# Optimization experiments

Hardware: AMD Instinct MI355X
Metric: run time of the kernel (lower is better)

## Reference

```python
import math
import jax, jax.numpy as jnp
import numpy as np

H = 16  # num_attention_heads
D = 64  # attention_head_size
ALPHA = 32.0  # PB-relax alpha


def setup_inputs() -> dict:
    key = jax.random.key(0)
    ks = jax.random.split(key, 8)
    B, S, C = 4, 1024, 1024
    scale = 1.0 / math.sqrt(C)
    return {
        "hidden_states": jax.random.normal(ks[0], (B, S, C), jnp.float32),
        "attention_mask": jnp.zeros((B, 1, 1, S), jnp.float32),
        "rel_pos": jax.random.normal(ks[1], (B, H, S, S), jnp.float32),
        "rel_2d_pos": jax.random.normal(ks[2], (B, H, S, S), jnp.float32),
        "Wq": jax.random.normal(ks[3], (C, C), jnp.float32) * scale,
        "bq": jnp.zeros((C,), jnp.float32),
        "Wk": jax.random.normal(ks[4], (C, C), jnp.float32) * scale,
        "bk": jnp.zeros((C,), jnp.float32),
        "Wv": jax.random.normal(ks[5], (C, C), jnp.float32) * scale,
        "bv": jnp.zeros((C,), jnp.float32),
    }


def _heads(x, B, S):
    # [B,S,C] -> [B,H,S,D]
    return x.reshape(B, S, H, D).transpose(0, 2, 1, 3)


def cogview_softmax(scores):
    # PB-relax: softmax(((s/alpha) - max(s/alpha)) * alpha)
    s = scores / ALPHA
    m = jnp.max(s, axis=-1, keepdims=True)
    return jax.nn.softmax((s - m) * ALPHA, axis=-1)


def reference(hidden_states, attention_mask, rel_pos, rel_2d_pos,
              Wq, bq, Wk, bk, Wv, bv):
    B, S, C = hidden_states.shape
    inv_sqrt_d = 1.0 / math.sqrt(D)
    # torch nn.Linear: y = x @ W.T + b; here W is stored as [out, in]
    q = _heads(hidden_states @ Wq.T + bq, B, S)  # [B,H,S,D]
    k = _heads(hidden_states @ Wk.T + bk, B, S)
    v = _heads(hidden_states @ Wv.T + bv, B, S)

    scores = jnp.einsum('bhqd,bhkd->bhqk', q * inv_sqrt_d, k)
    scores = scores + (rel_pos + rel_2d_pos) * inv_sqrt_d
    scores = scores + attention_mask  # broadcast [B,1,1,S]

    probs = cogview_softmax(scores)  # dropout prob = 0 (eval)
    ctx = jnp.einsum('bhqk,bhkd->bhqd', probs, v)
    ctx = ctx.transpose(0, 2, 1, 3).reshape(B, S, C)
    return ctx
```

## Files before the change

kernel.cpp:

```cpp
#include <hip/hip_runtime.h>
#include <hip/hip_bf16.h>

typedef __attribute__((ext_vector_type(8))) short bf16x8;
typedef __attribute__((ext_vector_type(4))) float f32x4;

#define LDSG(g, l) __builtin_amdgcn_global_load_lds(                      \
    (const __attribute__((address_space(1))) void*)(g),                   \
    (__attribute__((address_space(3))) void*)(l), 16, 0, 0)

#define LOG2E 1.44269504088896f
#define RELSC 0.180336880111112f

__global__ __launch_bounds__(256) void cvt_kernel(
    const float* __restrict__ hs,
    const float* __restrict__ wq, const float* __restrict__ wk,
    const float* __restrict__ wv,
    __hip_bfloat16* __restrict__ hbf, __hip_bfloat16* __restrict__ wbf)
{
  const int NH = (4 * 1024 * 1024) / 4;
  const int NW = (1024 * 1024) / 4;
  int i = blockIdx.x * 256 + threadIdx.x;
  float4 v;
  __hip_bfloat16* dst;
  if (i < NH) {
    v = ((const float4*)hs)[i];
    dst = hbf + (size_t)i * 4;
  } else {
    int j = i - NH;
    int which = j / NW, r = j - which * NW;
    const float* src = which == 0 ? wq : (which == 1 ? wk : wv);
    v = ((const float4*)src)[r];
    dst = wbf + (size_t)j * 4;
  }
  union { ushort4 u; __hip_bfloat16 b[4]; } o;
  o.b[0] = __float2bfloat16(v.x);
  o.b[1] = __float2bfloat16(v.y);
  o.b[2] = __float2bfloat16(v.z);
  o.b[3] = __float2bfloat16(v.w);
  *((ushort4*)dst) = o.u;
}

__global__ __launch_bounds__(256) void qkv_gemm(
    const __hip_bfloat16* __restrict__ A,
    const __hip_bfloat16* __restrict__ W,
    const float* __restrict__ bq, const float* __restrict__ bk,
    const float* __restrict__ bv,
    __hip_bfloat16* __restrict__ qo, __hip_bfloat16* __restrict__ ko,
    __hip_bfloat16* __restrict__ vo)
{
  const int K = 1024;
  __shared__ __hip_bfloat16 As[128 * 64];
  __shared__ __hip_bfloat16 Bs[128 * 64];
  const int bid = blockIdx.x;
  const int bm = bid & 31, bn = bid >> 5;
  const int m0 = bm * 128, n0 = bn * 128;
  const int tid = threadIdx.x, wid = tid >> 6, lane = tid & 63;
  const int wm = wid >> 1, wn = wid & 1;

  f32x4 acc[4][4] = {};

  const int srow = lane >> 3;
  const int schunk = (lane & 7) ^ srow;

  for (int k0 = 0; k0 < K; k0 += 64) {
#pragma unroll
    for (int p = 0; p < 4; ++p) {
      int r = (wid * 4 + p) * 8 + srow;
      LDSG(&A[(size_t)(m0 + r) * K + k0 + schunk * 8], &As[(wid * 4 + p) * 512]);
      LDSG(&W[(size_t)(n0 + r) * K + k0 + schunk * 8], &Bs[(wid * 4 + p) * 512]);
    }
    __syncthreads();
#pragma unroll
    for (int ks = 0; ks < 2; ++ks) {
      bf16x8 af[4], bfr[4];
#pragma unroll
      for (int mi = 0; mi < 4; ++mi) {
        int row = wm * 64 + mi * 16 + (lane & 15);
        int slot = (ks * 4 + (lane >> 4)) ^ (lane & 7);
        af[mi] = *(const bf16x8*)((const char*)As + row * 128 + slot * 16);
      }
#pragma unroll
      for (int ni = 0; ni < 4; ++ni) {
        int row = wn * 64 + ni * 16 + (lane & 15);
        int slot = (ks * 4 + (lane >> 4)) ^ (lane & 7);
        bfr[ni] = *(const bf16x8*)((const char*)Bs + row * 128 + slot * 16);
      }
#pragma unroll
      for (int mi = 0; mi < 4; ++mi)
#pragma unroll
        for (int ni = 0; ni < 4; ++ni)
          acc[mi][ni] = __builtin_amdgcn_mfma_f32_16x16x32_bf16(
              af[mi], bfr[ni], acc[mi][ni], 0, 0, 0);
    }
    __syncthreads();
  }

#pragma unroll
  for (int ni = 0; ni < 4; ++ni) {
    int n = n0 + wn * 64 + ni * 16 + (lane & 15);
    int which = n >> 10;
    int h = (n >> 6) & 15;
    int d = n & 63;
    const float* bias = which == 0 ? bq : (which == 1 ? bk : bv);
    float bval = bias[n & 1023];
    if (which == 0) {
#pragma unroll
      for (int mi = 0; mi < 4; ++mi) {
#pragma unroll
        for (int j = 0; j < 4; ++j) {
          int m = m0 + wm * 64 + mi * 16 + (lane >> 4) * 4 + j;
          int b = m >> 10, s = m & 1023;
          float val = (acc[mi][ni][j] + bval) * RELSC;
          qo[(((size_t)(b * 16 + h) << 10) + s) * 64 + d] = __float2bfloat16(val);
        }
      }
    } else if (which == 1) {
      int dks = d >> 5, dlg = (d >> 3) & 3, de = d & 7;
#pragma unroll
      for (int mi = 0; mi < 4; ++mi) {
#pragma unroll
        for (int j = 0; j < 4; ++j) {
          int m = m0 + wm * 64 + mi * 16 + (lane >> 4) * 4 + j;
          int b = m >> 10, s = m & 1023;
          size_t idx = ((((size_t)(b * 16 + h)) * 16 + (s >> 6)) * 512 +
                        (size_t)((dks * 4 + ((s >> 4) & 3)) * 64 + (s & 15) +
                                 16 * dlg)) * 8 + de;
          ko[idx] = __float2bfloat16(acc[mi][ni][j] + bval);
        }
      }
    } else {
      int dt = d >> 4, dl15 = d & 15;
#pragma unroll
      for (int mi = 0; mi < 4; ++mi) {
        int m = m0 + wm * 64 + mi * 16 + (lane >> 4) * 4;
        int b = m >> 10, k = m & 1023;
        int kt = k >> 6, kks = (k >> 5) & 1, klg = (k >> 3) & 3, ke = k & 7;
        union { ushort4 u; __hip_bfloat16 bb[4]; } o;
#pragma unroll
        for (int j = 0; j < 4; ++j)
          o.bb[j] = __float2bfloat16(acc[mi][ni][j] + bval);
        size_t idx = ((((size_t)(b * 16 + h)) * 16 + kt) * 512 +
                      (size_t)((kks * 4 + dt) * 64 + dl15 + 16 * klg)) * 8 + ke;
        *(ushort4*)&vo[idx] = o.u;
      }
    }
  }
}

__global__ __launch_bounds__(256, 2) void attn_kernel(
    const __hip_bfloat16* __restrict__ qg, const __hip_bfloat16* __restrict__ kf,
    const __hip_bfloat16* __restrict__ vf,
    const float* __restrict__ rel1, const float* __restrict__ rel2,
    const float* __restrict__ mask, float* __restrict__ out)
{
  __shared__ float Rbuf[4][2][2][16][64];
  __shared__ float Ml[1024];
  __shared__ __hip_bfloat16 Ps[4][16 * 64];

  const int bid = blockIdx.x;
  const int bh = bid & 63, qt = bid >> 6;
  const int b = bh >> 4, h = bh & 15;
  const int tid = threadIdx.x, wid = tid >> 6, lane = tid & 63;
  const int lg = lane >> 4, ln15 = lane & 15;
  const int r4 = lane >> 4, c15 = lane & 15;

  const size_t qbase = (size_t)bh << 16;
  const size_t fbase = (size_t)bh << 16;
  const int q0 = qt * 64 + wid * 16;

  {
    float4 mv = *(const float4*)&mask[((size_t)b << 10) + tid * 4];
    float4 sm;
    sm.x = mv.x * LOG2E - 32.0f; sm.y = mv.y * LOG2E - 32.0f;
    sm.z = mv.z * LOG2E - 32.0f; sm.w = mv.w * LOG2E - 32.0f;
    *(float4*)&Ml[tid * 4] = sm;
  }
  __syncthreads();

  bf16x8 qf[2];
  qf[0] = *(const bf16x8*)&qg[qbase + (size_t)(q0 + ln15) * 64 + lg * 8];
  qf[1] = *(const bf16x8*)&qg[qbase + (size_t)(q0 + ln15) * 64 + 32 + lg * 8];

  f32x4 accO[4] = {};
  float lrun = 0.f;

  const float* relw1 = rel1 + ((size_t)bh << 20);
  const float* relw2 = rel2 + ((size_t)bh << 20);

#define STAGE_REL(BUF, KB) do {                                             \
    _Pragma("unroll") for (int p = 0; p < 4; ++p) {                         \
      int rg = 4 * p + r4;                                                  \
      int cg = c15 ^ (rg & 7);                                              \
      LDSG(&relw1[(size_t)(q0 + rg) * 1024 + (KB) + cg * 4],                \
           &Rbuf[wid][BUF][0][4 * p][0]);                                   \
      LDSG(&relw2[(size_t)(q0 + rg) * 1024 + (KB) + cg * 4],                \
           &Rbuf[wid][BUF][1][4 * p][0]);                                   \
    } } while (0)

#define LOAD_K(KF_, KT) do {                                                \
    _Pragma("unroll") for (int i = 0; i < 8; ++i)                           \
      KF_[i] = *(const bf16x8*)&kf[fbase + (size_t)(KT) * 4096 + i * 512 +  \
                                   lane * 8];                               \
    } while (0)

#define LOAD_V(VF_, KT) do {                                                \
    _Pragma("unroll") for (int i = 0; i < 8; ++i)                           \
      VF_[i] = *(const bf16x8*)&vf[fbase + (size_t)(KT) * 4096 + i * 512 +  \
                                   lane * 8];                               \
    } while (0)

#define BODY(BUF, KT, DO_STAGE) do {                                        \
    bf16x8 kfr[8], vfr[8];                                                  \
    LOAD_K(kfr, KT);                                                        \
    LOAD_V(vfr, KT);                                                        \
    __builtin_amdgcn_sched_barrier(0);                                      \
    if (DO_STAGE) STAGE_REL((BUF) ^ 1, ((KT) + 1) * 64);                    \
    __builtin_amdgcn_sched_barrier(0);                                      \
    f32x4 st[4] = {};                                                       \
    _Pragma("unroll") for (int ks = 0; ks < 2; ++ks)                        \
      _Pragma("unroll") for (int ct = 0; ct < 4; ++ct)                      \
        st[ct] = __builtin_amdgcn_mfma_f32_16x16x32_bf16(                   \
            kfr[ks * 4 + ct], qf[ks], st[ct], 0, 0, 0);                     \
    asm volatile("s_waitcnt vmcnt(16)" ::: "memory");                       \
    __builtin_amdgcn_sched_barrier(0);                                      \
    float p[4][4];                                                          \
    _Pragma("unroll") for (int ct = 0; ct < 4; ++ct) {                      \
      int cc = ((ct * 4 + lg) ^ (ln15 & 7)) * 16;                           \
      float4 rv1 = *(const float4*)((const char*)&Rbuf[wid][BUF][0][0][0] + \
                                    ln15 * 256 + cc);                       \
      float4 rv2 = *(const float4*)((const char*)&Rbuf[wid][BUF][1][0][0] + \
                                    ln15 * 256 + cc);                       \
      float4 mv = *(const float4*)&Ml[(KT) * 64 + ct * 16 + lg * 4];        \
      _Pragma("unroll") for (int j = 0; j < 4; ++j) {                       \
        float sv = st[ct][j] +                                              \
                   RELSC * (((const float*)&rv1)[j] +                       \
                            ((const float*)&rv2)[j]) +                      \
                   ((const float*)&mv)[j];                                  \
        float e = __builtin_amdgcn_exp2f(sv);                               \
        p[ct][j] = e; lrun += e;                                            \
      }                                                                     \
    }                                                                       \
    __hip_bfloat16* Pw = &Ps[wid][0];                                       \
    _Pragma("unroll") for (int ct = 0; ct < 4; ++ct) {                      \
      union { ushort4 u; __hip_bfloat16 bb[4]; } w;                         \
      _Pragma("unroll") for (int j = 0; j < 4; ++j)                         \
        w.bb[j] = __float2bfloat16(p[ct][j]);                               \
      *(ushort4*)((char*)Pw + ln15 * 128 +                                  \
                  ((ct * 32 + lg * 8) ^ ((ln15 & 7) << 4))) = w.u;          \
    }                                                                       \
    bf16x8 pt[2];                                                           \
    pt[0] = *(const bf16x8*)((const char*)Pw + ln15 * 128 +                 \
                             ((lg * 16) ^ ((ln15 & 7) << 4)));              \
    pt[1] = *(const bf16x8*)((const char*)Pw + ln15 * 128 +                 \
                             ((64 + lg * 16) ^ ((ln15 & 7) << 4)));         \
    _Pragma("unroll") for (int ks = 0; ks < 2; ++ks)                        \
      _Pragma("unroll") for (int dt = 0; dt < 4; ++dt)                      \
        accO[dt] = __builtin_amdgcn_mfma_f32_16x16x32_bf16(                 \
            vfr[ks * 4 + dt], pt[ks], accO[dt], 0, 0, 0);                   \
  } while (0)

  STAGE_REL(0, 0);

  for (int t = 0; t < 7; ++t) {
    BODY(0, 2 * t, 1);
    BODY(1, 2 * t + 1, 1);
  }
  BODY(0, 14, 1);
  BODY(1, 15, 0);

  lrun += __shfl_xor(lrun, 16, 64);
  lrun += __shfl_xor(lrun, 32, 64);
  float rl = 1.0f / lrun;

#pragma unroll
  for (int dt = 0; dt < 4; ++dt) {
    float4 o;
    o.x = accO[dt][0] * rl;
    o.y = accO[dt][1] * rl;
    o.z = accO[dt][2] * rl;
    o.w = accO[dt][3] * rl;
    *(float4*)&out[((size_t)(b * 1024 + q0 + ln15)) * 1024 + h * 64 +
                   dt * 16 + lg * 4] = o;
  }
}

extern "C" void kernel_launch(void* const* d_in, const int* in_sizes, int n_in,
                              void* d_out, int out_size, void* d_ws,
                              size_t ws_size, hipStream_t stream) {
  const float* hs   = (const float*)d_in[0];
  const float* mask = (const float*)d_in[1];
  const float* rel1 = (const float*)d_in[2];
  const float* rel2 = (const float*)d_in[3];
  const float* Wq   = (const float*)d_in[4];
  const float* bq   = (const float*)d_in[5];
  const float* Wk   = (const float*)d_in[6];
  const float* bk   = (const float*)d_in[7];
  const float* Wv   = (const float*)d_in[8];
  const float* bv   = (const float*)d_in[9];

  char* ws = (char*)d_ws;
  __hip_bfloat16* hbf = (__hip_bfloat16*)(ws);
  __hip_bfloat16* wbf = (__hip_bfloat16*)(ws + 8388608);
  __hip_bfloat16* qb  = (__hip_bfloat16*)(ws + 14680064);
  __hip_bfloat16* kfb = (__hip_bfloat16*)(ws + 23068672);
  __hip_bfloat16* vfb = (__hip_bfloat16*)(ws + 31457280);

  cvt_kernel<<<7168, 256, 0, stream>>>(hs, Wq, Wk, Wv, hbf, wbf);
  qkv_gemm<<<768, 256, 0, stream>>>(hbf, wbf, bq, bk, bv, qb, kfb, vfb);
  attn_kernel<<<1024, 256, 0, stream>>>(qb, kfb, vfb, rel1, rel2, mask,
                                        (float*)d_out);
}
```

Measured before the change: 200.7 us.

## Split attention block into producer waves for rel-pos staging and consumer waves

Doubles the attention block to 512 threads. Four extra producer waves prefetch the rel_pos and rel_2d_pos tiles into double-buffered LDS with async global-to-LDS loads, while the four original waves only do the QK, softmax and PV math. The two groups hand off each 64-key step through a block-wide barrier, replacing the old per-wave software pipeline that issued its own staging loads and waited with a manual vmcnt. The intent is to overlap the heavy fp32 rel-pos streaming with the MFMA and exp work. The trade-offs are a barrier every iteration, and launch bounds of (512, 4) that cap VGPRs tightly, which may cause register spills in the consumer waves.

```diff
diff --git a/kernel.cpp b/kernel.cpp
--- a/kernel.cpp
+++ b/kernel.cpp
@@ -147,7 +147,7 @@
   }
 }
 
-__global__ __launch_bounds__(256, 2) void attn_kernel(
+__global__ __launch_bounds__(512, 4) void attn_kernel(
     const __hip_bfloat16* __restrict__ qg, const __hip_bfloat16* __restrict__ kf,
     const __hip_bfloat16* __restrict__ vf,
     const float* __restrict__ rel1, const float* __restrict__ rel2,
@@ -162,20 +162,52 @@
   const int b = bh >> 4, h = bh & 15;
   const int tid = threadIdx.x, wid = tid >> 6, lane = tid & 63;
   const int lg = lane >> 4, ln15 = lane & 15;
-  const int r4 = lane >> 4, c15 = lane & 15;
 
   const size_t qbase = (size_t)bh << 16;
   const size_t fbase = (size_t)bh << 16;
+
+  {
+    float2 mv = *(const float2*)&mask[((size_t)b << 10) + tid * 2];
+    float2 sm;
+    sm.x = mv.x * LOG2E - 32.0f;
+    sm.y = mv.y * LOG2E - 32.0f;
+    *(float2*)&Ml[tid * 2] = sm;
+  }
+
+  if (wid >= 4) {
+    const int cw = wid - 4;
+    const int q0c = qt * 64 + cw * 16;
+    const int r4 = lane >> 4, c15 = lane & 15;
+    const float* relw1 = rel1 + ((size_t)bh << 20);
+    const float* relw2 = rel2 + ((size_t)bh << 20);
+
+#pragma unroll
+    for (int p = 0; p < 4; ++p) {
+      int rg = 4 * p + r4;
+      int cg = c15 ^ (rg & 7);
+      LDSG(&relw1[(size_t)(q0c + rg) * 1024 + cg * 4], &Rbuf[cw][0][0][4 * p][0]);
+      LDSG(&relw2[(size_t)(q0c + rg) * 1024 + cg * 4], &Rbuf[cw][0][1][4 * p][0]);
+    }
+    __syncthreads();
+
+    for (int t = 0; t < 15; ++t) {
+      int buf = (t + 1) & 1;
+      int kb = (t + 1) * 64;
+#pragma unroll
+      for (int p = 0; p < 4; ++p) {
+        int rg = 4 * p + r4;
+        int cg = c15 ^ (rg & 7);
+        LDSG(&relw1[(size_t)(q0c + rg) * 1024 + kb + cg * 4],
+             &Rbuf[cw][buf][0][4 * p][0]);
+        LDSG(&relw2[(size_t)(q0c + rg) * 1024 + kb + cg * 4],
+             &Rbuf[cw][buf][1][4 * p][0]);
+      }
+      __syncthreads();
+    }
+    return;
+  }
+
   const int q0 = qt * 64 + wid * 16;
-
-  {
-    float4 mv = *(const float4*)&mask[((size_t)b << 10) + tid * 4];
-    float4 sm;
-    sm.x = mv.x * LOG2E - 32.0f; sm.y = mv.y * LOG2E - 32.0f;
-    sm.z = mv.z * LOG2E - 32.0f; sm.w = mv.w * LOG2E - 32.0f;
-    *(float4*)&Ml[tid * 4] = sm;
-  }
-  __syncthreads();
 
   bf16x8 qf[2];
   qf[0] = *(const bf16x8*)&qg[qbase + (size_t)(q0 + ln15) * 64 + lg * 8];
@@ -184,89 +216,69 @@
   f32x4 accO[4] = {};
   float lrun = 0.f;
 
-  const float* relw1 = rel1 + ((size_t)bh << 20);
-  const float* relw2 = rel2 + ((size_t)bh << 20);
-
-#define STAGE_REL(BUF, KB) do {                                             \
-    _Pragma("unroll") for (int p = 0; p < 4; ++p) {                         \
-      int rg = 4 * p + r4;                                                  \
-      int cg = c15 ^ (rg & 7);                                              \
-      LDSG(&relw1[(size_t)(q0 + rg) * 1024 + (KB) + cg * 4],                \
-           &Rbuf[wid][BUF][0][4 * p][0]);                                   \
-      LDSG(&relw2[(size_t)(q0 + rg) * 1024 + (KB) + cg * 4],                \
-           &Rbuf[wid][BUF][1][4 * p][0]);                                   \
-    } } while (0)
-
-#define LOAD_K(KF_, KT) do {                                                \
-    _Pragma("unroll") for (int i = 0; i < 8; ++i)                           \
-      KF_[i] = *(const bf16x8*)&kf[fbase + (size_t)(KT) * 4096 + i * 512 +  \
-                                   lane * 8];                               \
-    } while (0)
-
-#define LOAD_V(VF_, KT) do {                                                \
-    _Pragma("unroll") for (int i = 0; i < 8; ++i)                           \
-      VF_[i] = *(const bf16x8*)&vf[fbase + (size_t)(KT) * 4096 + i * 512 +  \
-                                   lane * 8];                               \
-    } while (0)
-
-#define BODY(BUF, KT, DO_STAGE) do {                                        \
-    bf16x8 kfr[8], vfr[8];                                                  \
-    LOAD_K(kfr, KT);                                                        \
-    LOAD_V(vfr, KT);                                                        \
-    __builtin_amdgcn_sched_barrier(0);                                      \
-    if (DO_STAGE) STAGE_REL((BUF) ^ 1, ((KT) + 1) * 64);                    \
-    __builtin_amdgcn_sched_barrier(0);                                      \
-    f32x4 st[4] = {};                                                       \
-    _Pragma("unroll") for (int ks = 0; ks < 2; ++ks)                        \
-      _Pragma("unroll") for (int ct = 0; ct < 4; ++ct)                      \
-        st[ct] = __builtin_amdgcn_mfma_f32_16x16x32_bf16(                   \
-            kfr[ks * 4 + ct], qf[ks], st[ct], 0, 0, 0);                     \
-    asm volatile("s_waitcnt vmcnt(16)" ::: "memory");                       \
-    __builtin_amdgcn_sched_barrier(0);                                      \
-    float p[4][4];                                                          \
-    _Pragma("unroll") for (int ct = 0; ct < 4; ++ct) {                      \
-      int cc = ((ct * 4 + lg) ^ (ln15 & 7)) * 16;                           \
-      float4 rv1 = *(const float4*)((const char*)&Rbuf[wid][BUF][0][0][0] + \
-                                    ln15 * 256 + cc);                       \
-      float4 rv2 = *(const float4*)((const char*)&Rbuf[wid][BUF][1][0][0] + \
-                                    ln15 * 256 + cc);                       \
-      float4 mv = *(const float4*)&Ml[(KT) * 64 + ct * 16 + lg * 4];        \
-      _Pragma("unroll") for (int j = 0; j < 4; ++j) {                       \
-        float sv = st[ct][j] +                                              \
-                   RELSC * (((const float*)&rv1)[j] +                       \
-                            ((const float*)&rv2)[j]) +                      \
-                   ((const float*)&mv)[j];                                  \
-        float e = __builtin_amdgcn_exp2f(sv);                               \
-        p[ct][j] = e; lrun += e;                                            \
-      }                                                                     \
-    }                                                                       \
-    __hip_bfloat16* Pw = &Ps[wid][0];                                       \
-    _Pragma("unroll") for (int ct = 0; ct < 4; ++ct) {                      \
-      union { ushort4 u; __hip_bfloat16 bb[4]; } w;                         \
-      _Pragma("unroll") for (int j = 0; j < 4; ++j)                         \
-        w.bb[j] = __float2bfloat16(p[ct][j]);                               \
-      *(ushort4*)((char*)Pw + ln15 * 128 +                                  \
-                  ((ct * 32 + lg * 8) ^ ((ln15 & 7) << 4))) = w.u;          \
-    }                                                                       \
-    bf16x8 pt[2];                                                           \
-    pt[0] = *(const bf16x8*)((const char*)Pw + ln15 * 128 +                 \
-                             ((lg * 16) ^ ((ln15 & 7) << 4)));              \
-    pt[1] = *(const bf16x8*)((const char*)Pw + ln15 * 128 +                 \
-                             ((64 + lg * 16) ^ ((ln15 & 7) << 4)));         \
-    _Pragma("unroll") for (int ks = 0; ks < 2; ++ks)                        \
-      _Pragma("unroll") for (int dt = 0; dt < 4; ++dt)                      \
-        accO[dt] = __builtin_amdgcn_mfma_f32_16x16x32_bf16(                 \
-            vfr[ks * 4 + dt], pt[ks], accO[dt], 0, 0, 0);                   \
-  } while (0)
-
-  STAGE_REL(0, 0);
-
-  for (int t = 0; t < 7; ++t) {
-    BODY(0, 2 * t, 1);
-    BODY(1, 2 * t + 1, 1);
-  }
-  BODY(0, 14, 1);
-  BODY(1, 15, 0);
+  __syncthreads();
+
+  for (int t = 0; t < 16; ++t) {
+    bf16x8 kfr[8], vfr[8];
+#pragma unroll
+    for (int i = 0; i < 8; ++i)
+      kfr[i] = *(const bf16x8*)&kf[fbase + (size_t)t * 4096 + i * 512 + lane * 8];
+#pragma unroll
+    for (int i = 0; i < 8; ++i)
+      vfr[i] = *(const bf16x8*)&vf[fbase + (size_t)t * 4096 + i * 512 + lane * 8];
+
+    f32x4 st[4] = {};
+#pragma unroll
+    for (int ks = 0; ks < 2; ++ks)
+#pragma unroll
+      for (int ct = 0; ct < 4; ++ct)
+        st[ct] = __builtin_amdgcn_mfma_f32_16x16x32_bf16(
+            kfr[ks * 4 + ct], qf[ks], st[ct], 0, 0, 0);
+
+    const char* Rb1 = (const char*)&Rbuf[wid][t & 1][0][0][0];
+    const char* Rb2 = (const char*)&Rbuf[wid][t & 1][1][0][0];
+    float p_[4][4];
+#pragma unroll
+    for (int ct = 0; ct < 4; ++ct) {
+      int cc = ((ct * 4 + lg) ^ (ln15 & 7)) * 16;
+      float4 rv1 = *(const float4*)(Rb1 + ln15 * 256 + cc);
+      float4 rv2 = *(const float4*)(Rb2 + ln15 * 256 + cc);
+      float4 mv = *(const float4*)&Ml[t * 64 + ct * 16 + lg * 4];
+#pragma unroll
+      for (int j = 0; j < 4; ++j) {
+        float sv = st[ct][j] +
+                   RELSC * (((const float*)&rv1)[j] + ((const float*)&rv2)[j]) +
+                   ((const float*)&mv)[j];
+        float e = __builtin_amdgcn_exp2f(sv);
+        p_[ct][j] = e;
+        lrun += e;
+      }
+    }
+
+    __hip_bfloat16* Pw = &Ps[wid][0];
+#pragma unroll
+    for (int ct = 0; ct < 4; ++ct) {
+      union { ushort4 u; __hip_bfloat16 bb[4]; } w;
+#pragma unroll
+      for (int j = 0; j < 4; ++j) w.bb[j] = __float2bfloat16(p_[ct][j]);
+      *(ushort4*)((char*)Pw + ln15 * 128 +
+                  ((ct * 32 + lg * 8) ^ ((ln15 & 7) << 4))) = w.u;
+    }
+    bf16x8 pt[2];
+    pt[0] = *(const bf16x8*)((const char*)Pw + ln15 * 128 +
+                             ((lg * 16) ^ ((ln15 & 7) << 4)));
+    pt[1] = *(const bf16x8*)((const char*)Pw + ln15 * 128 +
+                             ((64 + lg * 16) ^ ((ln15 & 7) << 4)));
+
+#pragma unroll
+    for (int ks = 0; ks < 2; ++ks)
+#pragma unroll
+      for (int dt = 0; dt < 4; ++dt)
+        accO[dt] = __builtin_amdgcn_mfma_f32_16x16x32_bf16(
+            vfr[ks * 4 + dt], pt[ks], accO[dt], 0, 0, 0);
+
+    if (t < 15) __syncthreads();
+  }
 
   lrun += __shfl_xor(lrun, 16, 64);
   lrun += __shfl_xor(lrun, 32, 64);
@@ -307,6 +319,6 @@
 
   cvt_kernel<<<7168, 256, 0, stream>>>(hs, Wq, Wk, Wv, hbf, wbf);
   qkv_gemm<<<768, 256, 0, stream>>>(hbf, wbf, bq, bk, bv, qb, kfb, vfb);
-  attn_kernel<<<1024, 256, 0, stream>>>(qb, kfb, vfb, rel1, rel2, mask,
+  attn_kernel<<<1024, 512, 0, stream>>>(qb, kfb, vfb, rel1, rel2, mask,
                                         (float*)d_out);
 }
```

Result: faster. 171.6 us (-14.5%).

## Warp-specialize attention: producer waves stage rel-pos tiles, consumer waves double-buffer K/V

Applied to the files above, without the earlier changes.

The attention block grows to 512 threads. Four producer waves fill the mask table and stream the two relative-position tiles into double-buffered LDS. Four consumer waves run the QK/softmax/PV math, prefetching the next K/V tile into a second register set. The two groups stay in step by matching barrier counts, so rel-pos staging leaves the compute waves' instruction stream. The tighter launch bounds (512 threads, 4 blocks) and the doubled K/V register footprint risk register spills, and LDS size probably caps how many blocks fit per CU.

```diff
diff --git a/kernel.cpp b/kernel.cpp
--- a/kernel.cpp
+++ b/kernel.cpp
@@ -147,7 +147,7 @@
   }
 }
 
-__global__ __launch_bounds__(256, 2) void attn_kernel(
+__global__ __launch_bounds__(512, 4) void attn_kernel(
     const __hip_bfloat16* __restrict__ qg, const __hip_bfloat16* __restrict__ kf,
     const __hip_bfloat16* __restrict__ vf,
     const float* __restrict__ rel1, const float* __restrict__ rel2,
@@ -162,89 +162,108 @@
   const int b = bh >> 4, h = bh & 15;
   const int tid = threadIdx.x, wid = tid >> 6, lane = tid & 63;
   const int lg = lane >> 4, ln15 = lane & 15;
-  const int r4 = lane >> 4, c15 = lane & 15;
 
   const size_t qbase = (size_t)bh << 16;
   const size_t fbase = (size_t)bh << 16;
+
+  if (wid >= 4) {
+    const int cw = wid - 4;
+    const int q0c = qt * 64 + cw * 16;
+    const int r4 = lane >> 4, c15 = lane & 15;
+    const float* relw1 = rel1 + ((size_t)bh << 20);
+    const float* relw2 = rel2 + ((size_t)bh << 20);
+
+    {
+      int i = cw * 64 + lane;
+      float4 mv = *(const float4*)&mask[((size_t)b << 10) + i * 4];
+      float4 sm;
+      sm.x = mv.x * LOG2E - 32.0f; sm.y = mv.y * LOG2E - 32.0f;
+      sm.z = mv.z * LOG2E - 32.0f; sm.w = mv.w * LOG2E - 32.0f;
+      *(float4*)&Ml[i * 4] = sm;
+    }
+
+#pragma unroll
+    for (int p = 0; p < 4; ++p) {
+      int rg = 4 * p + r4;
+      int cg = c15 ^ (rg & 7);
+      LDSG(&relw1[(size_t)(q0c + rg) * 1024 + cg * 4], &Rbuf[cw][0][0][4 * p][0]);
+      LDSG(&relw2[(size_t)(q0c + rg) * 1024 + cg * 4], &Rbuf[cw][0][1][4 * p][0]);
+    }
+    __syncthreads();
+
+    for (int t = 0; t < 15; ++t) {
+      int buf = (t + 1) & 1;
+      int kb = (t + 1) * 64;
+#pragma unroll
+      for (int p = 0; p < 4; ++p) {
+        int rg = 4 * p + r4;
+        int cg = c15 ^ (rg & 7);
+        LDSG(&relw1[(size_t)(q0c + rg) * 1024 + kb + cg * 4],
+             &Rbuf[cw][buf][0][4 * p][0]);
+        LDSG(&relw2[(size_t)(q0c + rg) * 1024 + kb + cg * 4],
+             &Rbuf[cw][buf][1][4 * p][0]);
+      }
+      __syncthreads();
+    }
+    return;
+  }
+
   const int q0 = qt * 64 + wid * 16;
-
-  {
-    float4 mv = *(const float4*)&mask[((size_t)b << 10) + tid * 4];
-    float4 sm;
-    sm.x = mv.x * LOG2E - 32.0f; sm.y = mv.y * LOG2E - 32.0f;
-    sm.z = mv.z * LOG2E - 32.0f; sm.w = mv.w * LOG2E - 32.0f;
-    *(float4*)&Ml[tid * 4] = sm;
-  }
-  __syncthreads();
 
   bf16x8 qf[2];
   qf[0] = *(const bf16x8*)&qg[qbase + (size_t)(q0 + ln15) * 64 + lg * 8];
   qf[1] = *(const bf16x8*)&qg[qbase + (size_t)(q0 + ln15) * 64 + 32 + lg * 8];
 
+  bf16x8 kA[8], vA[8], kB[8], vB[8];
+#pragma unroll
+  for (int i = 0; i < 8; ++i)
+    kA[i] = *(const bf16x8*)&kf[fbase + i * 512 + lane * 8];
+#pragma unroll
+  for (int i = 0; i < 8; ++i)
+    vA[i] = *(const bf16x8*)&vf[fbase + i * 512 + lane * 8];
+
   f32x4 accO[4] = {};
   float lrun = 0.f;
 
-  const float* relw1 = rel1 + ((size_t)bh << 20);
-  const float* relw2 = rel2 + ((size_t)bh << 20);
-
-#define STAGE_REL(BUF, KB) do {                                             \
-    _Pragma("unroll") for (int p = 0; p < 4; ++p) {                         \
-      int rg = 4 * p + r4;                                                  \
-      int cg = c15 ^ (rg & 7);                                              \
-      LDSG(&relw1[(size_t)(q0 + rg) * 1024 + (KB) + cg * 4],                \
-           &Rbuf[wid][BUF][0][4 * p][0]);                                   \
-      LDSG(&relw2[(size_t)(q0 + rg) * 1024 + (KB) + cg * 4],                \
-           &Rbuf[wid][BUF][1][4 * p][0]);                                   \
-    } } while (0)
-
-#define LOAD_K(KF_, KT) do {                                                \
-    _Pragma("unroll") for (int i = 0; i < 8; ++i)                           \
-      KF_[i] = *(const bf16x8*)&kf[fbase + (size_t)(KT) * 4096 + i * 512 +  \
-                                   lane * 8];                               \
-    } while (0)
-
-#define LOAD_V(VF_, KT) do {                                                \
-    _Pragma("unroll") for (int i = 0; i < 8; ++i)                           \
-      VF_[i] = *(const bf16x8*)&vf[fbase + (size_t)(KT) * 4096 + i * 512 +  \
-                                   lane * 8];                               \
-    } while (0)
-
-#define BODY(BUF, KT, DO_STAGE) do {                                        \
-    bf16x8 kfr[8], vfr[8];                                                  \
-    LOAD_K(kfr, KT);                                                        \
-    LOAD_V(vfr, KT);                                                        \
-    __builtin_amdgcn_sched_barrier(0);                                      \
-    if (DO_STAGE) STAGE_REL((BUF) ^ 1, ((KT) + 1) * 64);                    \
-    __builtin_amdgcn_sched_barrier(0);                                      \
+  __builtin_amdgcn_s_barrier();
+
+#define CBODY(KC, VC, KN, VN, T, PF) do {                                   \
+    if (PF) {                                                               \
+      _Pragma("unroll") for (int i = 0; i < 8; ++i)                         \
+        KN[i] = *(const bf16x8*)&kf[fbase + (size_t)((T) + 1) * 4096 +      \
+                                    i * 512 + lane * 8];                    \
+      _Pragma("unroll") for (int i = 0; i < 8; ++i)                         \
+        VN[i] = *(const bf16x8*)&vf[fbase + (size_t)((T) + 1) * 4096 +      \
+                                    i * 512 + lane * 8];                    \
+      __builtin_amdgcn_sched_barrier(0);                                    \
+    }                                                                       \
     f32x4 st[4] = {};                                                       \
     _Pragma("unroll") for (int ks = 0; ks < 2; ++ks)                        \
       _Pragma("unroll") for (int ct = 0; ct < 4; ++ct)                      \
         st[ct] = __builtin_amdgcn_mfma_f32_16x16x32_bf16(                   \
-            kfr[ks * 4 + ct], qf[ks], st[ct], 0, 0, 0);                     \
-    asm volatile("s_waitcnt vmcnt(16)" ::: "memory");                       \
-    __builtin_amdgcn_sched_barrier(0);                                      \
-    float p[4][4];                                                          \
+            KC[ks * 4 + ct], qf[ks], st[ct], 0, 0, 0);                      \
+    const char* Rb1 = (const char*)&Rbuf[wid][(T) & 1][0][0][0];            \
+    const char* Rb2 = (const char*)&Rbuf[wid][(T) & 1][1][0][0];            \
+    float p_[4][4];                                                         \
     _Pragma("unroll") for (int ct = 0; ct < 4; ++ct) {                      \
       int cc = ((ct * 4 + lg) ^ (ln15 & 7)) * 16;                           \
-      float4 rv1 = *(const float4*)((const char*)&Rbuf[wid][BUF][0][0][0] + \
-                                    ln15 * 256 + cc);                       \
-      float4 rv2 = *(const float4*)((const char*)&Rbuf[wid][BUF][1][0][0] + \
-                                    ln15 * 256 + cc);                       \
-      float4 mv = *(const float4*)&Ml[(KT) * 64 + ct * 16 + lg * 4];        \
+      float4 rv1 = *(const float4*)(Rb1 + ln15 * 256 + cc);                 \
+      float4 rv2 = *(const float4*)(Rb2 + ln15 * 256 + cc);                 \
+      float4 mv = *(const float4*)&Ml[(T) * 64 + ct * 16 + lg * 4];         \
       _Pragma("unroll") for (int j = 0; j < 4; ++j) {                       \
         float sv = st[ct][j] +                                              \
                    RELSC * (((const float*)&rv1)[j] +                       \
                             ((const float*)&rv2)[j]) +                      \
                    ((const float*)&mv)[j];                                  \
         float e = __builtin_amdgcn_exp2f(sv);                               \
-        p[ct][j] = e; lrun += e;                                            \
+        p_[ct][j] = e; lrun += e;                                           \
       }                                                                     \
     }                                                                       \
     __hip_bfloat16* Pw = &Ps[wid][0];                                       \
     _Pragma("unroll") for (int ct = 0; ct < 4; ++ct) {                      \
       union { ushort4 u; __hip_bfloat16 bb[4]; } w;                         \
       _Pragma("unroll") for (int j = 0; j < 4; ++j)                         \
-        w.bb[j] = __float2bfloat16(p[ct][j]);                               \
+        w.bb[j] = __float2bfloat16(p_[ct][j]);                              \
       *(ushort4*)((char*)Pw + ln15 * 128 +                                  \
                   ((ct * 32 + lg * 8) ^ ((ln15 & 7) << 4))) = w.u;          \
     }                                                                       \
@@ -256,17 +275,16 @@
     _Pragma("unroll") for (int ks = 0; ks < 2; ++ks)                        \
       _Pragma("unroll") for (int dt = 0; dt < 4; ++dt)                      \
         accO[dt] = __builtin_amdgcn_mfma_f32_16x16x32_bf16(                 \
-            vfr[ks * 4 + dt], pt[ks], accO[dt], 0, 0, 0);                   \
+            VC[ks * 4 + dt], pt[ks], accO[dt], 0, 0, 0);                    \
+    if ((T) < 15) __builtin_amdgcn_s_barrier();                             \
   } while (0)
 
-  STAGE_REL(0, 0);
-
   for (int t = 0; t < 7; ++t) {
-    BODY(0, 2 * t, 1);
-    BODY(1, 2 * t + 1, 1);
-  }
-  BODY(0, 14, 1);
-  BODY(1, 15, 0);
+    CBODY(kA, vA, kB, vB, 2 * t, 1);
+    CBODY(kB, vB, kA, vA, 2 * t + 1, 1);
+  }
+  CBODY(kA, vA, kB, vB, 14, 1);
+  CBODY(kB, vB, kA, vA, 15, 0);
 
   lrun += __shfl_xor(lrun, 16, 64);
   lrun += __shfl_xor(lrun, 32, 64);
@@ -307,6 +325,6 @@
 
   cvt_kernel<<<7168, 256, 0, stream>>>(hs, Wq, Wk, Wv, hbf, wbf);
   qkv_gemm<<<768, 256, 0, stream>>>(hbf, wbf, bq, bk, bv, qb, kfb, vfb);
-  attn_kernel<<<1024, 256, 0, stream>>>(qb, kfb, vfb, rel1, rel2, mask,
+  attn_kernel<<<1024, 512, 0, stream>>>(qb, kfb, vfb, rel1, rel2, mask,
                                         (float*)d_out);
 }
```

Result: slower. 408.4 us (+103.5%).
